# Kernel optimization log

Measured on AMD Instinct MI355X. Metric: run time of the kernel, lower is better.

## Reference

```python
import jax, jax.numpy as jnp
import numpy as np

D = 64  # hidden size

def _ffn2(x, w1, b1, w2, b2):
    # Linear -> ReLU -> Linear (no activation after last layer, matching FFN)
    return jax.nn.relu(x @ w1 + b1) @ w2 + b2

def setup_inputs() -> dict:
    key = jax.random.key(0)
    ks = jax.random.split(key, 40)
    B, NP, NY, NO = 512, 128, 1024, 256
    f32 = jnp.float32
    def n(k, sh, s=0.1):
        return (jax.random.normal(k, sh) * s).astype(f32)
    inp = {
        'pred_state': jax.random.normal(ks[0], (B, NP, 2), dtype=f32),
        'prey_state': jax.random.normal(ks[1], (B, NY, 2), dtype=f32),
        'obst_state': jax.random.normal(ks[2], (B, NO, 3), dtype=f32),
        'prey_is_alive': jax.random.randint(ks[3], (B, NY), 0, 2).astype(bool),
        'emb': n(ks[4], (3, D)),
        'e0_w1': n(ks[5], (2, D)), 'e0_b1': n(ks[6], (D,)),
        'e0_w2': n(ks[7], (D, D)), 'e0_b2': n(ks[8], (D,)),
        'e1_w1': n(ks[9], (2, D)), 'e1_b1': n(ks[10], (D,)),
        'e1_w2': n(ks[11], (D, D)), 'e1_b2': n(ks[12], (D,)),
        'e2_w1': n(ks[13], (3, D)), 'e2_b1': n(ks[14], (D,)),
        'e2_w2': n(ks[15], (D, D)), 'e2_b2': n(ks[16], (D,)),
        'wq': n(ks[17], (D, D)), 'bq': n(ks[18], (D,)),
        'wk': n(ks[19], (D, D)), 'bk': n(ks[20], (D,)),
        'wv': n(ks[21], (D, D)), 'bv': n(ks[22], (D,)),
        'wp': n(ks[23], (2, D)), 'bp': n(ks[24], (D,)),
        'wo': n(ks[25], (D, D)), 'bo': n(ks[26], (D,)),
        'n_w1': n(ks[27], (D, D)), 'n_b1': n(ks[28], (D,)),
        'n_w2': n(ks[29], (D, D)), 'n_b2': n(ks[30], (D,)),
        'n_w3': n(ks[31], (D, 1), s=0.01), 'n_b3': n(ks[32], (1,)),
    }
    return inp

def reference(pred_state, prey_state, obst_state, prey_is_alive, emb,
              e0_w1, e0_b1, e0_w2, e0_b2,
              e1_w1, e1_b1, e1_w2, e1_b2,
              e2_w1, e2_b1, e2_w2, e2_b2,
              wq, bq, wk, bk, wv, bv, wp, bp, wo, bo,
              n_w1, n_b1, n_w2, n_b2, n_w3, n_b3):
    # per-entity encoders + type embedding
    x_pred = _ffn2(pred_state, e0_w1, e0_b1, e0_w2, e0_b2) + emb[0]  # [B,NP,D]
    x_prey = _ffn2(prey_state, e1_w1, e1_b1, e1_w2, e1_b2) + emb[1]  # [B,NY,D]
    x_obst = _ffn2(obst_state, e2_w1, e2_b1, e2_w2, e2_b2) + emb[2]  # [B,NO,D]
    x = jnp.concatenate([x_pred, x_prey, x_obst], axis=1)            # [B,N,D]
    pos = jnp.concatenate([pred_state, prey_state, obst_state[..., :2]], axis=1)  # [B,N,2]
    # NOTE: original mask = zeros.unsqueeze(-1) & (...) is identically False -> no masking.
    q = x_pred @ wq + bq   # [B,NP,D]
    k = x @ wk + bk        # [B,N,D]
    v = x @ wv + bv        # [B,N,D]
    # relative positional key bias: pbias = (pos_q - pos_k) @ wp; q . pbias folded as below
    qp = q @ wp.T          # [B,NP,2]
    scale = np.float32(1.0 / np.sqrt(D))
    scores = (jnp.einsum('bqd,bkd->bqk', q, k)
              + jnp.einsum('bqc,bqc->bq', qp, pred_state)[..., None]
              - jnp.einsum('bqc,bkc->bqk', qp, pos)
              + (q @ bp)[..., None]) * scale          # [B,NP,N]
    a = jax.nn.softmax(scores, axis=-1)
    out = jnp.einsum('bqk,bkd->bqd', a, v) @ wo + bo  # [B,NP,D]
    # output FFN with final Tanh
    h = jax.nn.relu(out @ n_w1 + n_b1)
    h = jax.nn.relu(h @ n_w2 + n_b2)
    return jnp.tanh(h @ n_w3 + n_b3)                  # [B,NP,1]
```

## Files before the change

### kernel.cpp

```cpp
#include <hip/hip_runtime.h>
#include <math.h>

#define NB 512
#define NPQ 128
#define NY 1024
#define NO 256
#define NTOT 1408
#define SCALE_E 0.180336884f

typedef __attribute__((ext_vector_type(8))) short bf16x8;
typedef __attribute__((ext_vector_type(4))) float f32x4;

__device__ __forceinline__ unsigned short f2bf(float f) {
    unsigned int u = __float_as_uint(f);
    u += 0x7fffu + ((u >> 16) & 1u);
    return (unsigned short)(u >> 16);
}
__device__ __forceinline__ float bf2f(short s) {
    return __uint_as_float(((unsigned int)(unsigned short)s) << 16);
}

union U8  { bf16x8 v; unsigned long long u[2]; };
union U16 { bf16x8 v; uint4 u; };

__global__ __launch_bounds__(256) void k_prepA(
    const float* __restrict__ emb,  const float* __restrict__ e0b2,
    const float* __restrict__ e0w2, const float* __restrict__ wq,
    const float* __restrict__ bq,   const float* __restrict__ wp,
    const float* __restrict__ bp,   const float* __restrict__ bk,
    const float* __restrict__ wvv,  const float* __restrict__ bv,
    const float* __restrict__ wo,   const float* __restrict__ bo,
    const float* __restrict__ e1b2, const float* __restrict__ e1w2,
    const float* __restrict__ e2b2, const float* __restrict__ e2w2,
    const float* __restrict__ nw1,  const float* __restrict__ nw2,
    float* __restrict__ W2qG, float* __restrict__ WvoG,
    float* __restrict__ scqG, float* __restrict__ b0g0,
    float* __restrict__ bvo,  float* __restrict__ BEP,
    unsigned short* __restrict__ W2P, unsigned short* __restrict__ WHP)
{
    const int tid = threadIdx.x, blk = blockIdx.x;

    if (blk < 16) {
        const int idx = blk*256 + tid;
        const int h = idx >> 6, j = idx & 63;
        float s0 = 0.f, s1 = 0.f, s2 = 0.f, s3 = 0.f;
        #pragma unroll 4
        for (int e = 0; e < 64; e += 4) {
            s0 = fmaf(e0w2[h*64+e],   wq[(e  )*64+j], s0);
            s1 = fmaf(e0w2[h*64+e+1], wq[(e+1)*64+j], s1);
            s2 = fmaf(e0w2[h*64+e+2], wq[(e+2)*64+j], s2);
            s3 = fmaf(e0w2[h*64+e+3], wq[(e+3)*64+j], s3);
        }
        W2qG[idx] = (s0 + s1) + (s2 + s3);
    } else if (blk < 32) {
        const int idx = (blk-16)*256 + tid;
        const int e = idx >> 6, o = idx & 63;
        float s0 = 0.f, s1 = 0.f, s2 = 0.f, s3 = 0.f;
        #pragma unroll 4
        for (int d = 0; d < 64; d += 4) {
            s0 = fmaf(wvv[e*64+d],   wo[(d  )*64+o], s0);
            s1 = fmaf(wvv[e*64+d+1], wo[(d+1)*64+o], s1);
            s2 = fmaf(wvv[e*64+d+2], wo[(d+2)*64+o], s2);
            s3 = fmaf(wvv[e*64+d+3], wo[(d+3)*64+o], s3);
        }
        WvoG[idx] = (s0 + s1) + (s2 + s3);
    } else if (blk < 38) {
        const int idx = (blk-32)*256 + tid;
        if (idx < 1536) {
            const int t = idx >> 9, rem = idx & 511;
            const int mt = rem >> 7, rem2 = rem & 127;
            const int kh = rem2 >> 6, lane = rem2 & 63;
            const int quad = lane >> 4, lq = lane & 15;
            const float* w2 = (t == 0) ? e0w2 : ((t == 1) ? e1w2 : e2w2);
            unsigned short v[8];
            #pragma unroll
            for (int j = 0; j < 8; ++j)
                v[j] = f2bf(w2[(kh*32 + quad*8 + j)*64 + mt*16 + lq]);
            *(uint4*)&W2P[(size_t)idx*8] = make_uint4(
                (unsigned int)v[0] | ((unsigned int)v[1] << 16),
                (unsigned int)v[2] | ((unsigned int)v[3] << 16),
                (unsigned int)v[4] | ((unsigned int)v[5] << 16),
                (unsigned int)v[6] | ((unsigned int)v[7] << 16));
        }
    } else if (blk < 42) {
        const int idx = 512 + (blk-38)*256 + tid;
        const int l = idx >> 9, rem = idx & 511;
        const int mt = rem >> 7, rem2 = rem & 127;
        const int kh = rem2 >> 6, lane = rem2 & 63;
        const int quad = lane >> 4, lq = lane & 15;
        const float* W = (l == 1) ? nw1 : nw2;
        unsigned short v[8];
        #pragma unroll
        for (int j = 0; j < 8; ++j)
            v[j] = f2bf(W[(kh*32 + quad*8 + j)*64 + mt*16 + lq]);
        *(uint4*)&WHP[(size_t)idx*8] = make_uint4(
            (unsigned int)v[0] | ((unsigned int)v[1] << 16),
            (unsigned int)v[2] | ((unsigned int)v[3] << 16),
            (unsigned int)v[4] | ((unsigned int)v[5] << 16),
            (unsigned int)v[6] | ((unsigned int)v[7] << 16));
    } else {
        __shared__ float scq[64];
        if (tid < 64) {
            const int j = tid;
            float s = bq[j];
            for (int e = 0; e < 64; ++e) s += (e0b2[e] + emb[e]) * wq[e*64+j];
            scq[j] = s;
            scqG[j] = s;
        }
        if (tid >= 64 && tid < 128) {
            const int o = tid - 64;
            float s = bo[o];
            for (int d = 0; d < 64; ++d) s += bv[d] * wo[d*64+o];
            bvo[o] = s;
        }
        {
            const int i = tid - 64;
            if (i >= 64 && i < 256) {
                const int idx = i - 64;
                const int t = idx >> 6, d = idx & 63;
                const float* b2 = (t == 0) ? e0b2 : ((t == 1) ? e1b2 : e2b2);
                BEP[idx] = b2[d] + emb[t*64 + d];
            }
        }
        __syncthreads();
        if (tid == 0) {
            float s0 = 0.f, s1 = 0.f, s2 = 0.f;
            for (int j = 0; j < 64; ++j) {
                s0 += scq[j] * wp[j];
                s1 += scq[j] * wp[64+j];
                s2 += scq[j] * (bp[j] + bk[j]);
            }
            b0g0[0] = SCALE_E * s0;
            b0g0[1] = SCALE_E * s1;
            b0g0[2] = SCALE_E * s2;
        }
    }
}

__global__ __launch_bounds__(256) void k_prepB(
    const float* __restrict__ W2qG, const float* __restrict__ WvoG,
    const float* __restrict__ scqG,
    const float* __restrict__ wk, const float* __restrict__ wp,
    const float* __restrict__ bp, const float* __restrict__ bk,
    unsigned short* __restrict__ AqkP, unsigned short* __restrict__ P3P,
    float* __restrict__ a0, unsigned short* __restrict__ WHP)
{
    const int tid = threadIdx.x, blk = blockIdx.x;

    if (blk < 2) {
        const int idx = blk*256 + tid;
        const int fi = idx >> 6, lane = idx & 63;
        const int mt = fi >> 1, kh = fi & 1;
        const int quad = lane >> 4, lq = lane & 15;
        const int d = mt*16 + lq;
        unsigned short v[8];
        #pragma unroll
        for (int jj = 0; jj < 8; ++jj) {
            const int h = kh*32 + quad*8 + jj;
            float s0 = 0.f, s1 = 0.f, s2 = 0.f, s3 = 0.f;
            #pragma unroll 4
            for (int j = 0; j < 64; j += 4) {
                const float4 a = *(const float4*)&W2qG[h*64 + j];
                const float4 b = *(const float4*)&wk[d*64 + j];
                s0 = fmaf(a.x, b.x, s0); s1 = fmaf(a.y, b.y, s1);
                s2 = fmaf(a.z, b.z, s2); s3 = fmaf(a.w, b.w, s3);
            }
            v[jj] = f2bf(SCALE_E * ((s0 + s1) + (s2 + s3)));
        }
        *(uint4*)&AqkP[(size_t)idx*8] = make_uint4(
            (unsigned int)v[0] | ((unsigned int)v[1] << 16),
            (unsigned int)v[2] | ((unsigned int)v[3] << 16),
            (unsigned int)v[4] | ((unsigned int)v[5] << 16),
            (unsigned int)v[6] | ((unsigned int)v[7] << 16));
    } else if (blk == 2) {
        if (tid < 128) {
            const int idx = tid;
            const int kh = idx >> 6, lane = idx & 63;
            const int quad = lane >> 4, lq = lane & 15;
            unsigned short v[8];
            #pragma unroll
            for (int jj = 0; jj < 8; ++jj) {
                const int h = kh*32 + quad*8 + jj;
                float val = 0.f;
                if (lq == 0 || lq == 1) {
                    float s0 = 0.f, s1 = 0.f;
                    #pragma unroll 8
                    for (int j = 0; j < 64; j += 2) {
                        s0 = fmaf(W2qG[h*64+j],   wp[lq*64+j],   s0);
                        s1 = fmaf(W2qG[h*64+j+1], wp[lq*64+j+1], s1);
                    }
                    val = s0 + s1;
                } else if (lq == 2) {
                    float s0 = 0.f, s1 = 0.f;
                    #pragma unroll 8
                    for (int j = 0; j < 64; j += 2) {
                        s0 = fmaf(W2qG[h*64+j],   bp[j]   + bk[j],   s0);
                        s1 = fmaf(W2qG[h*64+j+1], bp[j+1] + bk[j+1], s1);
                    }
                    val = s0 + s1;
                }
                v[jj] = f2bf(SCALE_E * val);
            }
            *(uint4*)&P3P[(size_t)idx*8] = make_uint4(
                (unsigned int)v[0] | ((unsigned int)v[1] << 16),
                (unsigned int)v[2] | ((unsigned int)v[3] << 16),
                (unsigned int)v[4] | ((unsigned int)v[5] << 16),
                (unsigned int)v[6] | ((unsigned int)v[7] << 16));
        } else if (tid < 192) {
            const int d = tid - 128;
            float s0 = 0.f, s1 = 0.f, s2 = 0.f, s3 = 0.f;
            #pragma unroll 4
            for (int j = 0; j < 64; j += 4) {
                const float4 a = *(const float4*)&scqG[j];
                const float4 b = *(const float4*)&wk[d*64 + j];
                s0 = fmaf(a.x, b.x, s0); s1 = fmaf(a.y, b.y, s1);
                s2 = fmaf(a.z, b.z, s2); s3 = fmaf(a.w, b.w, s3);
            }
            a0[d] = SCALE_E * ((s0 + s1) + (s2 + s3));
        }
    } else {
        #pragma unroll
        for (int pass = 0; pass < 2; ++pass) {
            const int idx = pass*256 + tid;
            const int mt = idx >> 7, rem2 = idx & 127;
            const int kh = rem2 >> 6, lane = rem2 & 63;
            const int quad = lane >> 4, lq = lane & 15;
            unsigned short v[8];
            #pragma unroll
            for (int j = 0; j < 8; ++j)
                v[j] = f2bf(WvoG[(kh*32 + quad*8 + j)*64 + mt*16 + lq]);
            *(uint4*)&WHP[(size_t)idx*8] = make_uint4(
                (unsigned int)v[0] | ((unsigned int)v[1] << 16),
                (unsigned int)v[2] | ((unsigned int)v[3] << 16),
                (unsigned int)v[4] | ((unsigned int)v[5] << 16),
                (unsigned int)v[6] | ((unsigned int)v[7] << 16));
        }
    }
}

__global__ __launch_bounds__(256) void k_encq(
    const float* __restrict__ pred, const float* __restrict__ prey,
    const float* __restrict__ obst,
    const unsigned short* __restrict__ W2P, const float* __restrict__ BEP,
    const float* __restrict__ e0w1, const float* __restrict__ e0b1,
    const float* __restrict__ e1w1, const float* __restrict__ e1b1,
    const float* __restrict__ e2w1, const float* __restrict__ e2b1,
    const unsigned short* __restrict__ AqkP, const float* __restrict__ a0,
    const unsigned short* __restrict__ P3P,  const float* __restrict__ b0g0,
    unsigned short* __restrict__ X, float* __restrict__ POS,
    float* __restrict__ QT, float* __restrict__ QP, float* __restrict__ QC)
{
    const int tid = threadIdx.x, lane = tid & 63, w = tid >> 6;
    const int lq = lane & 15, quad = lane >> 4;
    __shared__ __align__(16) short sH[4][32][68];

    if (blockIdx.x < 1408) {
        const int blk = blockIdx.x;
        int type, lrow0, cin, lsh, nmask, nbase;
        const float *st, *w1, *b1;
        if (blk < 128)       { type=0; lrow0=blk*512;         st=pred; w1=e0w1; b1=e0b1; cin=2; lsh=7;  nmask=NPQ-1; nbase=0; }
        else if (blk < 1152) { type=1; lrow0=(blk-128)*512;   st=prey; w1=e1w1; b1=e1b1; cin=2; lsh=10; nmask=NY-1;  nbase=NPQ; }
        else                 { type=2; lrow0=(blk-1152)*512;  st=obst; w1=e2w1; b1=e2b1; cin=3; lsh=8;  nmask=NO-1;  nbase=NPQ+NY; }

        bf16x8 wfrag[4][2];
        #pragma unroll
        for (int mt = 0; mt < 4; ++mt)
            #pragma unroll
            for (int kh = 0; kh < 2; ++kh)
                wfrag[mt][kh] = *(const bf16x8*)&W2P[(size_t)(((type*4 + mt)*2 + kh)*64 + lane)*8];

        float4 be[4];
        #pragma unroll
        for (int mt = 0; mt < 4; ++mt)
            be[mt] = *(const float4*)&BEP[type*64 + mt*16 + quad*4];

        float b1v[2][8], w0v[2][8], w1v[2][8], w2v[2][8];
        #pragma unroll
        for (int kh = 0; kh < 2; ++kh) {
            const int k0 = kh*32 + quad*8;
            *(float4*)&b1v[kh][0] = *(const float4*)&b1[k0];
            *(float4*)&b1v[kh][4] = *(const float4*)&b1[k0+4];
            *(float4*)&w0v[kh][0] = *(const float4*)&w1[k0];
            *(float4*)&w0v[kh][4] = *(const float4*)&w1[k0+4];
            *(float4*)&w1v[kh][0] = *(const float4*)&w1[64+k0];
            *(float4*)&w1v[kh][4] = *(const float4*)&w1[64+k0+4];
            if (cin == 3) {
                *(float4*)&w2v[kh][0] = *(const float4*)&w1[128+k0];
                *(float4*)&w2v[kh][4] = *(const float4*)&w1[128+k0+4];
            }
        }

        #pragma unroll
        for (int k = 0; k < 4; ++k) {
            const int i = tid*4 + k;
            const int r = i >> 1, c = i & 1;
            const int lr = lrow0 + r;
            const int pb = lr >> lsh, n = nbase + (lr & nmask);
            POS[((size_t)pb*NTOT + n)*2 + c] = st[(size_t)lr*cin + c];
        }

        for (int rt = 0; rt < 8; ++rt) {
            const int lr = lrow0 + w*128 + rt*16 + lq;
            float s0, s1, s2 = 0.f;
            if (cin == 2) {
                const float2 sv = *(const float2*)&st[(size_t)lr*2];
                s0 = sv.x; s1 = sv.y;
            } else {
                const float2 sv = *(const float2*)&st[(size_t)lr*3];
                s0 = sv.x; s1 = sv.y; s2 = st[(size_t)lr*3 + 2];
            }
            bf16x8 hb[2];
            #pragma unroll
            for (int kh = 0; kh < 2; ++kh)
                #pragma unroll
                for (int j = 0; j < 8; ++j) {
                    float a = b1v[kh][j] + s0*w0v[kh][j] + s1*w1v[kh][j];
                    if (cin == 3) a += s2*w2v[kh][j];
                    hb[kh][j] = (short)f2bf(fmaxf(a, 0.f));
                }

            f32x4 acc[4];
            #pragma unroll
            for (int mt = 0; mt < 4; ++mt) acc[mt] = (f32x4){0.f,0.f,0.f,0.f};
            #pragma unroll
            for (int mt = 0; mt < 4; ++mt) {
                acc[mt] = __builtin_amdgcn_mfma_f32_16x16x32_bf16(wfrag[mt][0], hb[0], acc[mt], 0, 0, 0);
                acc[mt] = __builtin_amdgcn_mfma_f32_16x16x32_bf16(wfrag[mt][1], hb[1], acc[mt], 0, 0, 0);
            }

            const int bb = lr >> lsh, n = nbase + (lr & nmask);
            unsigned short* xbase = X + ((size_t)bb*NTOT + n)*64;
            #pragma unroll
            for (int mt = 0; mt < 4; ++mt) {
                const unsigned int u0 = (unsigned int)f2bf(acc[mt][0] + be[mt].x)
                                      | ((unsigned int)f2bf(acc[mt][1] + be[mt].y) << 16);
                const unsigned int u1 = (unsigned int)f2bf(acc[mt][2] + be[mt].z)
                                      | ((unsigned int)f2bf(acc[mt][3] + be[mt].w) << 16);
                *(uint2*)(xbase + mt*16 + quad*4) = make_uint2(u0, u1);
            }
        }
    } else {
        const int b = blockIdx.x - 1408;
        const float w1r0 = e0w1[lane], w1r1 = e0w1[64+lane], b1r = e0b1[lane];
        {
            const float* sp = pred + ((size_t)b*NPQ + w*32)*2;
            #pragma unroll
            for (int r = 0; r < 32; ++r) {
                const float a = b1r + sp[2*r]*w1r0 + sp[2*r+1]*w1r1;
                sH[w][r][lane] = (short)f2bf(fmaxf(a, 0.f));
            }
        }

        bf16x8 wfrag[4][2], a3[2];
        #pragma unroll
        for (int mt = 0; mt < 4; ++mt)
            #pragma unroll
            for (int kh = 0; kh < 2; ++kh)
                wfrag[mt][kh] = *(const bf16x8*)&AqkP[(size_t)((mt*2 + kh)*64 + lane)*8];
        #pragma unroll
        for (int kh = 0; kh < 2; ++kh)
            a3[kh] = *(const bf16x8*)&P3P[(size_t)(kh*64 + lane)*8];

        float4 a0r[4];
        #pragma unroll
        for (int mt = 0; mt < 4; ++mt) a0r[mt] = *(const float4*)&a0[mt*16 + quad*4];
        const float c0 = b0g0[0], c1 = b0g0[1], c2 = b0g0[2];

        __syncthreads();

        for (int bt = 0; bt < 2; ++bt) {
            U8 hb0, hb1;
            const short* hp = &sH[w][bt*16 + lq][0];
            hb0.u[0] = *(const unsigned long long*)(hp + quad*8);
            hb0.u[1] = *(const unsigned long long*)(hp + quad*8 + 4);
            hb1.u[0] = *(const unsigned long long*)(hp + 32 + quad*8);
            hb1.u[1] = *(const unsigned long long*)(hp + 32 + quad*8 + 4);

            f32x4 acc[4], acc3;
            #pragma unroll
            for (int mt = 0; mt < 4; ++mt) acc[mt] = (f32x4){0.f,0.f,0.f,0.f};
            acc3 = (f32x4){0.f,0.f,0.f,0.f};
            #pragma unroll
            for (int mt = 0; mt < 4; ++mt) {
                acc[mt] = __builtin_amdgcn_mfma_f32_16x16x32_bf16(wfrag[mt][0], hb0.v, acc[mt], 0, 0, 0);
                acc[mt] = __builtin_amdgcn_mfma_f32_16x16x32_bf16(wfrag[mt][1], hb1.v, acc[mt], 0, 0, 0);
            }
            acc3 = __builtin_amdgcn_mfma_f32_16x16x32_bf16(a3[0], hb0.v, acc3, 0, 0, 0);
            acc3 = __builtin_amdgcn_mfma_f32_16x16x32_bf16(a3[1], hb1.v, acc3, 0, 0, 0);

            const int row = b*NPQ + w*32 + bt*16 + lq;
            #pragma unroll
            for (int mt = 0; mt < 4; ++mt) {
                *(float4*)&QT[(size_t)row*64 + mt*16 + quad*4] = make_float4(
                    acc[mt][0] + a0r[mt].x, acc[mt][1] + a0r[mt].y,
                    acc[mt][2] + a0r[mt].z, acc[mt][3] + a0r[mt].w);
            }
            if (quad == 0) {
                const float qp0 = acc3[0] + c0, qp1 = acc3[1] + c1, qs = acc3[2] + c2;
                const float p0 = pred[(size_t)row*2], p1 = pred[(size_t)row*2 + 1];
                QP[(size_t)row*2]     = qp0;
                QP[(size_t)row*2 + 1] = qp1;
                QC[row] = qp0*p0 + qp1*p1 + qs;
            }
        }
    }
}

__global__ __launch_bounds__(256) void k_attn(
    const unsigned short* __restrict__ X, const float* __restrict__ POS,
    const float* __restrict__ QT, const float* __restrict__ QP,
    const float* __restrict__ QC,
    const unsigned short* __restrict__ WHP,
    const float* __restrict__ bvo, const float* __restrict__ nb1,
    const float* __restrict__ nb2,
    const float* __restrict__ nw3, const float* __restrict__ nb3,
    float* __restrict__ OUT)
{
    const int tid = threadIdx.x, b = blockIdx.x;
    const int w = tid >> 6, lane = tid & 63, lq = lane & 15, quad = lane >> 4;

    __shared__ __align__(16) char smem[34816 + 256];
    short (*sXc)[64][68] = (short (*)[64][68])(smem);
    short (*sP )[32][68] = (short (*)[32][68])(smem + 17408);
    short (*sA )[68]     = (short (*)[68])(smem);
    short (*sB )[68]     = (short (*)[68])(smem + 17408);
    float* sw3           = (float*)(smem + 34816);

    bf16x8 aq[2][2];
    #pragma unroll
    for (int qt = 0; qt < 2; ++qt) {
        const float* qrow = QT + ((size_t)b*NPQ + w*32 + qt*16 + lq)*64;
        #pragma unroll
        for (int kh = 0; kh < 2; ++kh)
            #pragma unroll
            for (int j = 0; j < 8; ++j)
                aq[qt][kh][j] = (short)f2bf(qrow[kh*32 + quad*8 + j]);
    }

    float qp0r[2][4], qp1r[2][4], lacc[2][4];
    f32x4 qcv[2];
    f32x4 O[2][4];
    #pragma unroll
    for (int qt = 0; qt < 2; ++qt)
        #pragma unroll
        for (int i = 0; i < 4; ++i) {
            const size_t g = (size_t)b*NPQ + w*32 + qt*16 + quad*4 + i;
            qcv[qt][i]  = QC[g];
            qp0r[qt][i] = -QP[2*g];
            qp1r[qt][i] = -QP[2*g+1];
            lacc[qt][i] = 0.f;
        }
    #pragma unroll
    for (int qt = 0; qt < 2; ++qt)
        #pragma unroll
        for (int nt = 0; nt < 4; ++nt) O[qt][nt] = (f32x4){0.f,0.f,0.f,0.f};

    const int skey = tid & 63, sd0 = (tid >> 6) * 16;

    for (int kt = 0; kt < 22; ++kt) {
        const int par = kt & 1;

        const unsigned short* gx = X + ((size_t)b*NTOT + kt*64 + skey)*64 + sd0;
        const uint4 t0 = *(const uint4*)(gx);
        const uint4 t1 = *(const uint4*)(gx + 8);

        uint4 bxa[4], bxb[4];
        float2 posv[4];
        #pragma unroll
        for (int nt = 0; nt < 4; ++nt) {
            const unsigned short* xrow = X + ((size_t)b*NTOT + kt*64 + nt*16 + lq)*64;
            bxa[nt]  = *(const uint4*)(xrow + quad*8);
            bxb[nt]  = *(const uint4*)(xrow + 32 + quad*8);
            posv[nt] = *(const float2*)&POS[((size_t)b*NTOT + kt*64 + nt*16 + lq)*2];
        }

        if (kt > 0) {
            const int pb = par ^ 1;
            #pragma unroll
            for (int kc = 0; kc < 2; ++kc) {
                U8 pa[2];
                #pragma unroll
                for (int qt = 0; qt < 2; ++qt) {
                    const short* pp = &sP[w][qt*16 + lq][kc*32 + quad*8];
                    pa[qt].u[0] = *(const unsigned long long*)pp;
                    pa[qt].u[1] = *(const unsigned long long*)(pp + 4);
                }
                #pragma unroll
                for (int nt = 0; nt < 4; ++nt) {
                    U8 bv;
                    const short* xp = &sXc[pb][nt*16 + lq][kc*32 + quad*8];
                    bv.u[0] = *(const unsigned long long*)xp;
                    bv.u[1] = *(const unsigned long long*)(xp + 4);
                    O[0][nt] = __builtin_amdgcn_mfma_f32_16x16x32_bf16(pa[0].v, bv.v, O[0][nt], 0, 0, 0);
                    O[1][nt] = __builtin_amdgcn_mfma_f32_16x16x32_bf16(pa[1].v, bv.v, O[1][nt], 0, 0, 0);
                }
            }
        }

        __builtin_amdgcn_sched_barrier(0);

        #pragma unroll
        for (int nt = 0; nt < 4; ++nt) {
            U16 bx0, bx1;
            bx0.u = bxa[nt];
            bx1.u = bxb[nt];
            const float pos0 = posv[nt].x;
            const float pos1 = posv[nt].y;
            #pragma unroll
            for (int qt = 0; qt < 2; ++qt) {
                f32x4 sa = qcv[qt];
                sa = __builtin_amdgcn_mfma_f32_16x16x32_bf16(aq[qt][0], bx0.v, sa, 0, 0, 0);
                sa = __builtin_amdgcn_mfma_f32_16x16x32_bf16(aq[qt][1], bx1.v, sa, 0, 0, 0);
                #pragma unroll
                for (int i = 0; i < 4; ++i) {
                    float s = sa[i];
                    s = fmaf(qp0r[qt][i], pos0, s);
                    s = fmaf(qp1r[qt][i], pos1, s);
                    const float p = exp2f(s);
                    lacc[qt][i] += p;
                    sP[w][qt*16 + quad*4 + i][nt*16 + lq] = (short)f2bf(p);
                }
            }
        }

        {
            unsigned short tmp[16];
            *(uint4*)tmp = t0; *(uint4*)(tmp+8) = t1;
            #pragma unroll
            for (int j = 0; j < 16; ++j) sXc[par][sd0+j][skey] = (short)tmp[j];
        }

        __syncthreads();
    }

    {
        #pragma unroll
        for (int kc = 0; kc < 2; ++kc) {
            U8 pa[2];
            #pragma unroll
            for (int qt = 0; qt < 2; ++qt) {
                const short* pp = &sP[w][qt*16 + lq][kc*32 + quad*8];
                pa[qt].u[0] = *(const unsigned long long*)pp;
                pa[qt].u[1] = *(const unsigned long long*)(pp + 4);
            }
            #pragma unroll
            for (int nt = 0; nt < 4; ++nt) {
                U8 bv;
                const short* xp = &sXc[1][nt*16 + lq][kc*32 + quad*8];
                bv.u[0] = *(const unsigned long long*)xp;
                bv.u[1] = *(const unsigned long long*)(xp + 4);
                O[0][nt] = __builtin_amdgcn_mfma_f32_16x16x32_bf16(pa[0].v, bv.v, O[0][nt], 0, 0, 0);
                O[1][nt] = __builtin_amdgcn_mfma_f32_16x16x32_bf16(pa[1].v, bv.v, O[1][nt], 0, 0, 0);
            }
        }
    }

    __syncthreads();

    #pragma unroll
    for (int qt = 0; qt < 2; ++qt)
        #pragma unroll
        for (int i = 0; i < 4; ++i) {
            #pragma unroll
            for (int off = 1; off < 16; off <<= 1)
                lacc[qt][i] += __shfl_xor(lacc[qt][i], off);
            const float rl = 1.f / lacc[qt][i];
            const int row = w*32 + qt*16 + quad*4 + i;
            #pragma unroll
            for (int nt = 0; nt < 4; ++nt)
                sA[row][nt*16 + lq] = (short)f2bf(O[qt][nt][i] * rl);
        }
    if (tid < 64) sw3[tid] = nw3[tid];
    __syncthreads();

    const float* Bs[3] = {bvo, nb1, nb2};
    for (int l = 0; l < 3; ++l) {
        bf16x8 wfrag[4][2];
        #pragma unroll
        for (int mt = 0; mt < 4; ++mt)
            #pragma unroll
            for (int kh = 0; kh < 2; ++kh)
                wfrag[mt][kh] = *(const bf16x8*)&WHP[(size_t)(((l*4 + mt)*2 + kh)*64 + lane)*8];
        const float* Bb = Bs[l];
        float be[4][4];
        #pragma unroll
        for (int mt = 0; mt < 4; ++mt)
            #pragma unroll
            for (int i = 0; i < 4; ++i) be[mt][i] = Bb[mt*16 + quad*4 + i];

        short (*src)[68] = (l & 1) ? sB : sA;
        short (*dst)[68] = (l & 1) ? sA : sB;
        const bool doRelu = (l >= 1);

        for (int bt = 0; bt < 2; ++bt) {
            U8 hb0, hb1;
            const short* hp = &src[w*32 + bt*16 + lq][0];
            hb0.u[0] = *(const unsigned long long*)(hp + quad*8);
            hb0.u[1] = *(const unsigned long long*)(hp + quad*8 + 4);
            hb1.u[0] = *(const unsigned long long*)(hp + 32 + quad*8);
            hb1.u[1] = *(const unsigned long long*)(hp + 32 + quad*8 + 4);

            f32x4 acc[4];
            #pragma unroll
            for (int mt = 0; mt < 4; ++mt) acc[mt] = (f32x4){0.f,0.f,0.f,0.f};
            #pragma unroll
            for (int mt = 0; mt < 4; ++mt) {
                acc[mt] = __builtin_amdgcn_mfma_f32_16x16x32_bf16(wfrag[mt][0], hb0.v, acc[mt], 0, 0, 0);
                acc[mt] = __builtin_amdgcn_mfma_f32_16x16x32_bf16(wfrag[mt][1], hb1.v, acc[mt], 0, 0, 0);
            }
            const int row = w*32 + bt*16 + lq;
            #pragma unroll
            for (int mt = 0; mt < 4; ++mt) {
                float v0 = acc[mt][0] + be[mt][0];
                float v1 = acc[mt][1] + be[mt][1];
                float v2 = acc[mt][2] + be[mt][2];
                float v3 = acc[mt][3] + be[mt][3];
                if (doRelu) {
                    v0 = fmaxf(v0, 0.f); v1 = fmaxf(v1, 0.f);
                    v2 = fmaxf(v2, 0.f); v3 = fmaxf(v3, 0.f);
                }
                const unsigned int u0 = (unsigned int)f2bf(v0) | ((unsigned int)f2bf(v1) << 16);
                const unsigned int u1 = (unsigned int)f2bf(v2) | ((unsigned int)f2bf(v3) << 16);
                *(uint2*)&dst[row][mt*16 + quad*4] = make_uint2(u0, u1);
            }
        }
        __syncthreads();
    }

    if (tid < 128) {
        const int row = tid;
        float acc = nb3[0];
        #pragma unroll 16
        for (int d = 0; d < 64; ++d) acc += bf2f(sB[row][d]) * sw3[d];
        OUT[(size_t)b*NPQ + row] = tanhf(acc);
    }
}

extern "C" void kernel_launch(void* const* d_in, const int* in_sizes, int n_in,
                              void* d_out, int out_size, void* d_ws, size_t ws_size,
                              hipStream_t stream)
{
    const float* pred = (const float*)d_in[0];
    const float* prey = (const float*)d_in[1];
    const float* obst = (const float*)d_in[2];
    const float* emb  = (const float*)d_in[4];
    const float* e0w1 = (const float*)d_in[5];
    const float* e0b1 = (const float*)d_in[6];
    const float* e0w2 = (const float*)d_in[7];
    const float* e0b2 = (const float*)d_in[8];
    const float* e1w1 = (const float*)d_in[9];
    const float* e1b1 = (const float*)d_in[10];
    const float* e1w2 = (const float*)d_in[11];
    const float* e1b2 = (const float*)d_in[12];
    const float* e2w1 = (const float*)d_in[13];
    const float* e2b1 = (const float*)d_in[14];
    const float* e2w2 = (const float*)d_in[15];
    const float* e2b2 = (const float*)d_in[16];
    const float* wq  = (const float*)d_in[17];
    const float* bq  = (const float*)d_in[18];
    const float* wk  = (const float*)d_in[19];
    const float* bk  = (const float*)d_in[20];
    const float* wvv = (const float*)d_in[21];
    const float* bv  = (const float*)d_in[22];
    const float* wp  = (const float*)d_in[23];
    const float* bp  = (const float*)d_in[24];
    const float* wo  = (const float*)d_in[25];
    const float* bo  = (const float*)d_in[26];
    const float* nw1 = (const float*)d_in[27];
    const float* nb1 = (const float*)d_in[28];
    const float* nw2 = (const float*)d_in[29];
    const float* nb2 = (const float*)d_in[30];
    const float* nw3 = (const float*)d_in[31];
    const float* nb3 = (const float*)d_in[32];

    char* ws = (char*)d_ws;
    unsigned short* X = (unsigned short*)ws;
    float* F    = (float*)(ws + 92274688);
    float* POS  = F;
    float* QT   = POS + 1441792;
    float* QP   = QT  + 4194304;
    float* QC   = QP  + 131072;
    float* a0   = QC  + 65536;
    float* b0g0 = a0  + 64;
    float* bvo  = b0g0 + 4;
    float* BEP  = bvo + 64;
    float* W2qG = BEP + 192;
    float* WvoG = W2qG + 4096;
    float* scqG = WvoG + 4096;
    unsigned short* W2P  = (unsigned short*)(scqG + 64);
    unsigned short* AqkP = W2P + 12288;
    unsigned short* P3P  = AqkP + 4096;
    unsigned short* WHP  = P3P + 1024;

    k_prepA<<<43, 256, 0, stream>>>(emb, e0b2, e0w2, wq, bq, wp, bp, bk,
        wvv, bv, wo, bo, e1b2, e1w2, e2b2, e2w2, nw1, nw2,
        W2qG, WvoG, scqG, b0g0, bvo, BEP, W2P, WHP);
    k_prepB<<<4, 256, 0, stream>>>(W2qG, WvoG, scqG, wk, wp, bp, bk,
        AqkP, P3P, a0, WHP);
    k_encq<<<1920, 256, 0, stream>>>(pred, prey, obst, W2P, BEP,
        e0w1, e0b1, e1w1, e1b1, e2w1, e2b1,
        AqkP, a0, P3P, b0g0, X, POS, QT, QP, QC);
    k_attn<<<512, 256, 0, stream>>>(X, POS, QT, QP, QC,
        WHP, bvo, nb1, nb2, nw3, nb3, (float*)d_out);
}
```

Baseline: 253.4 us.

## Prefetch next key tile into LDS and read score operands from shared memory

The attention kernel now stages the next 64-key tile of X into shared memory one iteration ahead. It keeps a row-major double buffer for the score MFMA and a triple-buffered transposed copy for the P·V MFMA. Previously each warp fetched its score operands straight from global memory on every iteration, duplicating loads across warps. Shared memory grows from about 35 KB to about 61 KB per block, which can lower occupancy, and the tile load, ring-buffer indexing and tail handling all change together.

```diff
diff --git a/kernel.cpp b/kernel.cpp
--- a/kernel.cpp
+++ b/kernel.cpp
@@ -419,12 +419,13 @@
     const int tid = threadIdx.x, b = blockIdx.x;
     const int w = tid >> 6, lane = tid & 63, lq = lane & 15, quad = lane >> 4;
 
-    __shared__ __align__(16) char smem[34816 + 256];
-    short (*sXc)[64][68] = (short (*)[64][68])(smem);
-    short (*sP )[32][68] = (short (*)[32][68])(smem + 17408);
-    short (*sA )[68]     = (short (*)[68])(smem);
-    short (*sB )[68]     = (short (*)[68])(smem + 17408);
-    float* sw3           = (float*)(smem + 34816);
+    __shared__ __align__(16) char smem[61184];
+    short (*sRowX)[64][68] = (short (*)[64][68])(smem);
+    short (*sXcT)[64][68]  = (short (*)[64][68])(smem + 17408);
+    short (*sP )[32][68]   = (short (*)[32][68])(smem + 43520);
+    short (*sA )[68]       = (short (*)[68])(smem);
+    short (*sB )[68]       = (short (*)[68])(smem + 17408);
+    float* sw3             = (float*)(smem + 60928);
 
     bf16x8 aq[2][2];
     #pragma unroll
@@ -457,25 +458,41 @@
 
     const int skey = tid & 63, sd0 = (tid >> 6) * 16;
 
+    {
+        const unsigned short* gx = X + ((size_t)b*NTOT + skey)*64 + sd0;
+        const uint4 p0 = *(const uint4*)(gx);
+        const uint4 p1 = *(const uint4*)(gx + 8);
+        *(uint4*)&sRowX[0][skey][sd0]     = p0;
+        *(uint4*)&sRowX[0][skey][sd0 + 8] = p1;
+        unsigned short tmp[16];
+        *(uint4*)tmp = p0; *(uint4*)(tmp+8) = p1;
+        #pragma unroll
+        for (int j = 0; j < 16; ++j) sXcT[0][sd0+j][skey] = (short)tmp[j];
+        __syncthreads();
+    }
+
     for (int kt = 0; kt < 22; ++kt) {
-        const int par = kt & 1;
-
-        const unsigned short* gx = X + ((size_t)b*NTOT + kt*64 + skey)*64 + sd0;
-        const uint4 t0 = *(const uint4*)(gx);
-        const uint4 t1 = *(const uint4*)(gx + 8);
-
-        uint4 bxa[4], bxb[4];
+        const int par  = kt & 1;
+        const int pvS  = (kt + 2) % 3;
+        const int stS  = (kt + 1) % 3;
+
+        uint4 t0 = make_uint4(0,0,0,0), t1 = make_uint4(0,0,0,0);
+        if (kt < 21) {
+            const unsigned short* gx = X + ((size_t)b*NTOT + (kt+1)*64 + skey)*64 + sd0;
+            t0 = *(const uint4*)(gx);
+            t1 = *(const uint4*)(gx + 8);
+        }
+
         float2 posv[4];
+        U16 bxa[4], bxb[4];
         #pragma unroll
         for (int nt = 0; nt < 4; ++nt) {
-            const unsigned short* xrow = X + ((size_t)b*NTOT + kt*64 + nt*16 + lq)*64;
-            bxa[nt]  = *(const uint4*)(xrow + quad*8);
-            bxb[nt]  = *(const uint4*)(xrow + 32 + quad*8);
             posv[nt] = *(const float2*)&POS[((size_t)b*NTOT + kt*64 + nt*16 + lq)*2];
+            bxa[nt].u = *(const uint4*)&sRowX[par][nt*16 + lq][quad*8];
+            bxb[nt].u = *(const uint4*)&sRowX[par][nt*16 + lq][32 + quad*8];
         }
 
         if (kt > 0) {
-            const int pb = par ^ 1;
             #pragma unroll
             for (int kc = 0; kc < 2; ++kc) {
                 U8 pa[2];
@@ -488,7 +505,7 @@
                 #pragma unroll
                 for (int nt = 0; nt < 4; ++nt) {
                     U8 bv;
-                    const short* xp = &sXc[pb][nt*16 + lq][kc*32 + quad*8];
+                    const short* xp = &sXcT[pvS][nt*16 + lq][kc*32 + quad*8];
                     bv.u[0] = *(const unsigned long long*)xp;
                     bv.u[1] = *(const unsigned long long*)(xp + 4);
                     O[0][nt] = __builtin_amdgcn_mfma_f32_16x16x32_bf16(pa[0].v, bv.v, O[0][nt], 0, 0, 0);
@@ -501,16 +518,13 @@
 
         #pragma unroll
         for (int nt = 0; nt < 4; ++nt) {
-            U16 bx0, bx1;
-            bx0.u = bxa[nt];
-            bx1.u = bxb[nt];
             const float pos0 = posv[nt].x;
             const float pos1 = posv[nt].y;
             #pragma unroll
             for (int qt = 0; qt < 2; ++qt) {
                 f32x4 sa = qcv[qt];
-                sa = __builtin_amdgcn_mfma_f32_16x16x32_bf16(aq[qt][0], bx0.v, sa, 0, 0, 0);
-                sa = __builtin_amdgcn_mfma_f32_16x16x32_bf16(aq[qt][1], bx1.v, sa, 0, 0, 0);
+                sa = __builtin_amdgcn_mfma_f32_16x16x32_bf16(aq[qt][0], bxa[nt].v, sa, 0, 0, 0);
+                sa = __builtin_amdgcn_mfma_f32_16x16x32_bf16(aq[qt][1], bxb[nt].v, sa, 0, 0, 0);
                 #pragma unroll
                 for (int i = 0; i < 4; ++i) {
                     float s = sa[i];
@@ -523,11 +537,13 @@
             }
         }
 
-        {
+        if (kt < 21) {
+            *(uint4*)&sRowX[par^1][skey][sd0]     = t0;
+            *(uint4*)&sRowX[par^1][skey][sd0 + 8] = t1;
             unsigned short tmp[16];
             *(uint4*)tmp = t0; *(uint4*)(tmp+8) = t1;
             #pragma unroll
-            for (int j = 0; j < 16; ++j) sXc[par][sd0+j][skey] = (short)tmp[j];
+            for (int j = 0; j < 16; ++j) sXcT[stS][sd0+j][skey] = (short)tmp[j];
         }
 
         __syncthreads();
@@ -546,7 +562,7 @@
             #pragma unroll
             for (int nt = 0; nt < 4; ++nt) {
                 U8 bv;
-                const short* xp = &sXc[1][nt*16 + lq][kc*32 + quad*8];
+                const short* xp = &sXcT[0][nt*16 + lq][kc*32 + quad*8];
                 bv.u[0] = *(const unsigned long long*)xp;
                 bv.u[1] = *(const unsigned long long*)(xp + 4);
                 O[0][nt] = __builtin_amdgcn_mfma_f32_16x16x32_bf16(pa[0].v, bv.v, O[0][nt], 0, 0, 0);
```

After: 265.9 us. 4.9% more time.
